# Kernel tuning notes

Hardware: AMD Instinct MI355X
Metric: run time of the kernel (lower is better)

Reference implementation:

```python
import jax, jax.numpy as jnp
import numpy as np
from jax.scipy.special import logsumexp

NEG = -1e9  # soft -inf for log-domain boundaries (avoids NaN grads)


def _viterbi_score(theta, A):
    """Smooth (logsumexp-operator) 3-state affine-gap HMM Viterbi score.

    theta: [B, N, M, 3] emission scores, state order (m, x, y)
    A:     [B, N, M, 3, 3] transition scores A[..., u, v] = u -> v
    Returns per-batch terminal score [B].
    Recurrence:
      V[i,j,m] = theta[i,j,m] + LSE_u(V[i-1,j-1,u] + A[i,j,u,m])
      V[i,j,x] = theta[i,j,x] + LSE_u(V[i-1,j  ,u] + A[i,j,u,x])
      V[i,j,y] = theta[i,j,y] + LSE_u(V[i  ,j-1,u] + A[i,j,u,y])
    The y-state within-row recurrence is a log-domain linear recurrence
    solved with an associative scan (wavefront-free row parallelism).
    """
    B, N, Mlen, S = theta.shape
    dt = theta.dtype

    def combine(e1, e2):
        a1, b1 = e1
        a2, b2 = e2
        return a1 + a2, jnp.logaddexp(b1 + a2, b2)

    # V row over j = 0..M (j=0 is boundary column); start state at (0,0,m)
    V0 = jnp.full((B, Mlen + 1, S), NEG, dt).at[:, 0, 0].set(0.0)
    neg_col = jnp.full((B, 1), NEG, dt)

    def row_step(Vprev, xs):
        th, Aij = xs                      # [B,M,3], [B,M,3,3]
        prev_diag = Vprev[:, :-1]         # V[i-1, j-1, :] for j=1..M
        prev_up = Vprev[:, 1:]            # V[i-1, j,   :]
        Vm = th[..., 0] + logsumexp(prev_diag + Aij[..., 0], axis=-1)
        Vx = th[..., 1] + logsumexp(prev_up + Aij[..., 1], axis=-1)
        # y-state: V_y[j] = logaddexp(a[j] + V_y[j-1], b[j])
        Vm_l = jnp.concatenate([neg_col, Vm[:, :-1]], axis=1)  # V[i,j-1,m]
        Vx_l = jnp.concatenate([neg_col, Vx[:, :-1]], axis=1)  # V[i,j-1,x]
        a = Aij[..., 2, 2] + th[..., 2]
        b = th[..., 2] + jnp.logaddexp(Vm_l + Aij[..., 0, 2],
                                       Vx_l + Aij[..., 1, 2])
        _, Vy = jax.lax.associative_scan(combine, (a, b), axis=1)
        Vrow = jnp.concatenate(
            [jnp.full((B, 1, S), NEG, dt),
             jnp.stack([Vm, Vx, Vy], axis=-1)], axis=1)
        return Vrow, None

    theta_t = jnp.moveaxis(theta, 1, 0)   # [N,B,M,3]
    A_t = jnp.moveaxis(A, 1, 0)           # [N,B,M,3,3]
    Vlast, _ = jax.lax.scan(row_step, V0, (theta_t, A_t))
    return logsumexp(Vlast[:, -1], axis=-1)  # [B]


def setup_inputs() -> dict:
    key = jax.random.key(0)
    ks = jax.random.split(key, 4)
    B, N, M, d, S = 8, 512, 512, 256, 3
    sc = jnp.float32(0.1)
    return {
        "zx": jax.random.normal(ks[0], (B, N, d, S), jnp.float32) * sc,
        "zy": jax.random.normal(ks[1], (B, M, d, S), jnp.float32) * sc,
        "gx": jax.random.normal(ks[2], (B, N, d, S), jnp.float32) * sc,
        "gy": jax.random.normal(ks[3], (B, M, d, S), jnp.float32) * sc,
    }


def reference(zx, zy, gx, gy):
    # HMM3Aligner.contract (no softplus/logsigmoid in the 3-state override)
    theta = jnp.einsum('bids,bjds->bijs', zx, zy)      # [B,N,M,3]
    A = jnp.einsum('bidu,bjdv->bijuv', gx, gy)         # [B,N,M,3,3]
    # hmm.decode: posterior alignment = grad of smooth Viterbi score w.r.t. theta
    aln = jax.grad(lambda th: _viterbi_score(th, A).sum())(theta)
    return aln  # [B,N,M,3]
```

## Files before the change

### kernel.cpp

```cpp
#include <hip/hip_runtime.h>
#include <cstdint>

#define DEVI __device__ __forceinline__

#define NEGC  (-1.0e9f)
#define NEGID (-2.0e9f)

DEVI float lse2f(float p, float q){
  float m = fmaxf(p, q);
  return m + __logf(__expf(p - m) + __expf(q - m));
}
DEVI float lse3f(float a, float b, float c){
  float m = fmaxf(fmaxf(a, b), c);
  return m + __logf(__expf(a - m) + __expf(b - m) + __expf(c - m));
}

DEVI void bar_raw(){
  asm volatile("s_waitcnt lgkmcnt(0)" ::: "memory");
  __builtin_amdgcn_s_barrier();
  asm volatile("" ::: "memory");
}
DEVI void bar_full(){
  asm volatile("s_waitcnt vmcnt(0) lgkmcnt(0)" ::: "memory");
  __builtin_amdgcn_s_barrier();
  asm volatile("" ::: "memory");
}

DEVI void gld_lds16(const float* g, float* l){
  __builtin_amdgcn_global_load_lds(
    (const __attribute__((address_space(1))) unsigned int*)(uintptr_t)g,
    (__attribute__((address_space(3))) unsigned int*)(uintptr_t)l,
    16, 0, 0);
}
DEVI void stage8(const float* g, float* l, int nchunks, int wid, int lane){
  for (int c = wid; c < nchunks; c += 8)
    gld_lds16(g + (size_t)c*256 + lane*4, l + (size_t)c*256);
}

__global__ __launch_bounds__(256) void k_gemm_th(
    const float* __restrict__ zx, const float* __restrict__ zy, float* __restrict__ th){
  const int b  = blockIdx.z;
  const int i0 = blockIdx.y * 64, j0 = blockIdx.x * 64;
  const int tid = threadIdx.x;
  const int tx = tid & 15, ty = tid >> 4;
  __shared__ __align__(16) float xs[16*3*64];
  __shared__ __align__(16) float ys[16*3*64];
  const float* xb = zx + ((size_t)b*512 + i0) * 768;
  const float* yb = zy + ((size_t)b*512 + j0) * 768;
  float acc[3][4][4] = {};
  for (int k = 0; k < 256; k += 16) {
    #pragma unroll
    for (int p = 0; p < 3; ++p) {
      int q = tid + p*256;
      int row = q / 12, f4 = q % 12;
      float4 xv = *(const float4*)(xb + (size_t)row*768 + k*3 + f4*4);
      float4 yv = *(const float4*)(yb + (size_t)row*768 + k*3 + f4*4);
      const float* xe = (const float*)&xv;
      const float* ye = (const float*)&yv;
      #pragma unroll
      for (int e = 0; e < 4; ++e) {
        int idx = f4*4 + e;
        xs[idx*64 + row] = xe[e];
        ys[idx*64 + row] = ye[e];
      }
    }
    __syncthreads();
    #pragma unroll
    for (int dd = 0; dd < 16; ++dd) {
      float4 xa[3], yv2[3];
      #pragma unroll
      for (int s = 0; s < 3; ++s) {
        xa[s]  = *(const float4*)&xs[(dd*3 + s)*64 + ty*4];
        yv2[s] = *(const float4*)&ys[(dd*3 + s)*64 + tx*4];
      }
      #pragma unroll
      for (int s = 0; s < 3; ++s)
        #pragma unroll
        for (int a2 = 0; a2 < 4; ++a2)
          #pragma unroll
          for (int c = 0; c < 4; ++c)
            acc[s][a2][c] += ((const float*)&xa[s])[a2] * ((const float*)&yv2[s])[c];
    }
    __syncthreads();
  }
  #pragma unroll
  for (int s = 0; s < 3; ++s)
    #pragma unroll
    for (int a2 = 0; a2 < 4; ++a2) {
      float4 v = make_float4(acc[s][a2][0], acc[s][a2][1], acc[s][a2][2], acc[s][a2][3]);
      *(float4*)(th + (((size_t)b*512 + i0 + ty*4 + a2)*3 + s)*512 + j0 + tx*4) = v;
    }
}

__global__ __launch_bounds__(256) void k_gemm_A(
    const float* __restrict__ gx, const float* __restrict__ gy, float* __restrict__ Ag){
  const int b  = blockIdx.z;
  const int i0 = blockIdx.y * 32, j0 = blockIdx.x * 32;
  const int tid = threadIdx.x;
  const int tx = tid & 15, ty = tid >> 4;
  __shared__ __align__(16) float xs[32*3*32];
  __shared__ __align__(16) float ys[32*3*32];
  const float* xb = gx + ((size_t)b*512 + i0) * 768;
  const float* yb = gy + ((size_t)b*512 + j0) * 768;
  float acc[3][3][2][2] = {};
  for (int k = 0; k < 256; k += 32) {
    #pragma unroll
    for (int p = 0; p < 3; ++p) {
      int q = tid + p*256;
      int row = q / 24, f4 = q % 24;
      float4 xv = *(const float4*)(xb + (size_t)row*768 + k*3 + f4*4);
      float4 yv = *(const float4*)(yb + (size_t)row*768 + k*3 + f4*4);
      const float* xe = (const float*)&xv;
      const float* ye = (const float*)&yv;
      #pragma unroll
      for (int e = 0; e < 4; ++e) {
        int idx = f4*4 + e;
        xs[idx*32 + row] = xe[e];
        ys[idx*32 + row] = ye[e];
      }
    }
    __syncthreads();
    #pragma unroll
    for (int dd = 0; dd < 32; ++dd) {
      float2 ga[3], gb[3];
      #pragma unroll
      for (int u = 0; u < 3; ++u) ga[u] = *(const float2*)&xs[(dd*3 + u)*32 + ty*2];
      #pragma unroll
      for (int v = 0; v < 3; ++v) gb[v] = *(const float2*)&ys[(dd*3 + v)*32 + tx*2];
      #pragma unroll
      for (int u = 0; u < 3; ++u)
        #pragma unroll
        for (int v = 0; v < 3; ++v) {
          acc[u][v][0][0] += ga[u].x * gb[v].x;
          acc[u][v][0][1] += ga[u].x * gb[v].y;
          acc[u][v][1][0] += ga[u].y * gb[v].x;
          acc[u][v][1][1] += ga[u].y * gb[v].y;
        }
    }
    __syncthreads();
  }
  #pragma unroll
  for (int u = 0; u < 3; ++u)
    #pragma unroll
    for (int v = 0; v < 3; ++v)
      #pragma unroll
      for (int a2 = 0; a2 < 2; ++a2) {
        float2 w; w.x = acc[u][v][a2][0]; w.y = acc[u][v][a2][1];
        *(float2*)(Ag + ((((size_t)b*512 + i0 + ty*2 + a2)*3 + v)*3 + u)*512 + j0 + tx*2) = w;
      }
}

__global__ __launch_bounds__(512) void k_fwd(
    const float* __restrict__ th, const float* __restrict__ Ag,
    float* __restrict__ V, float* __restrict__ score){
  const int b = blockIdx.x;
  const int tid = threadIdx.x;
  const int lane = tid & 63, wid = tid >> 6;
  __shared__ __align__(16) float th_s[2][1536];
  __shared__ __align__(16) float A_s[2][4608];
  __shared__ float Vbuf[2][3*513];
  __shared__ float wag[8][2];
  const float* thb = th + (size_t)b * 512 * 1536;
  const float* Ab  = Ag + (size_t)b * 512 * 4608;
  float*       Vb  = V  + (size_t)b * 512 * 1536;

  for (int kk = tid; kk < 2*3*513; kk += 512) (&Vbuf[0][0])[kk] = NEGC;
  __syncthreads();
  if (tid == 0) Vbuf[0][0] = 0.f;
  stage8(thb, th_s[0], 6, wid, lane);
  stage8(Ab,  A_s[0], 18, wid, lane);
  bar_full();

  int pv = 0;
  for (int i = 1; i <= 512; ++i) {
    const int bc = (i - 1) & 1;
    if (i < 512) {
      stage8(thb + (size_t)i*1536, th_s[i & 1], 6, wid, lane);
      stage8(Ab  + (size_t)i*4608, A_s[i & 1], 18, wid, lane);
    }
    const float* ths = th_s[bc];
    const float* As  = A_s[bc];
    float* Vp = Vbuf[pv];
    float* Vc = Vbuf[pv ^ 1];
    const int tj = tid, j = tid + 1;

    float thm = ths[tj], thx = ths[512 + tj], thy = ths[1024 + tj];
    float vd0 = Vp[tj],     vd1 = Vp[513 + tj],     vd2 = Vp[2*513 + tj];
    float vu0 = Vp[tj + 1], vu1 = Vp[513 + tj + 1], vu2 = Vp[2*513 + tj + 1];
    float Vm = thm + lse3f(vd0 + As[tj],        vd1 + As[512 + tj],  vd2 + As[1024 + tj]);
    float Vx = thx + lse3f(vu0 + As[1536 + tj], vu1 + As[2048 + tj], vu2 + As[2560 + tj]);
    Vc[j] = Vm; Vc[513 + j] = Vx;
    if (tid == 0) { Vc[0] = NEGC; Vc[513] = NEGC; Vc[2*513] = NEGC; }
    bar_raw();
    float Vml = Vc[tj];
    float Vxl = Vc[513 + tj];
    float a  = As[4096 + tj] + thy;
    float bb = thy + lse2f(Vml + As[3072 + tj], Vxl + As[3584 + tj]);
    #pragma unroll
    for (int st = 1; st < 64; st <<= 1) {
      float ao = __shfl_up(a,  st, 64);
      float bo = __shfl_up(bb, st, 64);
      if (lane >= st) { bb = lse2f(bo + a, bb); a += ao; }
    }
    if (lane == 63) { wag[wid][0] = a; wag[wid][1] = bb; }
    bar_raw();
    float pb = NEGID;
    for (int w = 0; w < wid; ++w) pb = lse2f(pb + wag[w][0], wag[w][1]);
    float Vy = lse2f(pb + a, bb);
    Vc[2*513 + j] = Vy;
    float* Vr = Vb + (size_t)(i - 1) * 1536;
    Vr[tj] = Vm; Vr[512 + tj] = Vx; Vr[1024 + tj] = Vy;
    bar_full();
    pv ^= 1;
  }
  if (tid == 0) {
    float* Vl = Vbuf[pv];
    score[b] = lse3f(Vl[512], Vl[513 + 512], Vl[2*513 + 512]);
  }
}

__global__ __launch_bounds__(512) void k_bwd(
    const float* __restrict__ th, const float* __restrict__ Ag,
    const float* __restrict__ V, const float* __restrict__ score,
    float* __restrict__ out){
  const int b = blockIdx.x;
  const int tid = threadIdx.x;
  const int lane = tid & 63, wid = tid >> 6;
  __shared__ __align__(16) float th_s[3][1536];
  __shared__ __align__(16) float A_s[3][4608];
  __shared__ __align__(16) float Vls[3][1536];
  __shared__ float Eb[2][3*514];
  __shared__ float wag[8][2];
  const float* thb = th + (size_t)b * 512 * 1536;
  const float* Ab  = Ag + (size_t)b * 512 * 4608;
  const float* Vb  = V  + (size_t)b * 512 * 1536;
  float* ob = out + (size_t)b * 512 * 512 * 3;

  for (int kk = tid; kk < 2*3*514; kk += 512) (&Eb[0][0])[kk] = 0.f;
  stage8(thb + (size_t)511*1536, th_s[1], 6, wid, lane);
  stage8(Ab  + (size_t)511*4608, A_s[1], 18, wid, lane);
  stage8(Vb  + (size_t)511*1536, Vls[2], 6, wid, lane);
  float sc = score[b];
  bar_full();

  int ce = 0;
  for (int i = 512; i >= 1; --i) {
    if (i >= 2) {
      stage8(thb + (size_t)(i-2)*1536, th_s[(i-2)%3], 6, wid, lane);
      stage8(Ab  + (size_t)(i-2)*4608, A_s[(i-2)%3], 18, wid, lane);
      stage8(Vb  + (size_t)(i-2)*1536, Vls[(i-1)%3], 6, wid, lane);
    }
    const float* thN = th_s[(i-1)%3];
    const float* AN  = A_s[(i-1)%3];
    const float* thK = th_s[i%3];
    const float* AK  = A_s[i%3];
    const float* Vc  = Vls[i%3];
    const float* Vn  = Vls[(i+1)%3];
    const float* E1  = Eb[ce ^ 1];
    float* Ec = Eb[ce];
    const int tj = tid;
    const bool hasN = (i < 512);
    const bool hasJ = (tid < 511);
    const int  c1 = hasJ ? tid + 1 : tid;

    float v0 = Vc[tj], v1 = Vc[512 + tj], v2 = Vc[1024 + tj];
    float vyr = hasJ ? Vc[1024 + c1] : 0.f;
    float vnm = Vn[c1];
    float vnx = Vn[512 + tj];
    float e1m = E1[tid + 2];
    float e1x = E1[514 + tid + 1];
    float thT1 = thK[c1], thT2 = thK[512 + tj], thT3 = thN[1024 + c1];

    float w;
    w = (hasN && hasJ) ? e1m * __expf(v0 + AK[c1]       + thT1 - vnm) : 0.f;
    float D0 = w + (hasN ? e1x * __expf(v0 + AK[1536 + tj] + thT2 - vnx) : 0.f);
    float wy0 = hasJ ? __expf(v0 + AN[3072 + c1] + thT3 - vyr) : 0.f;
    w = (hasN && hasJ) ? e1m * __expf(v1 + AK[512 + c1] + thT1 - vnm) : 0.f;
    float D1 = w + (hasN ? e1x * __expf(v1 + AK[2048 + tj] + thT2 - vnx) : 0.f);
    float wy1 = hasJ ? __expf(v1 + AN[3584 + c1] + thT3 - vyr) : 0.f;
    w = (hasN && hasJ) ? e1m * __expf(v2 + AK[1024 + c1] + thT1 - vnm) : 0.f;
    float D2 = w + (hasN ? e1x * __expf(v2 + AK[2560 + tj] + thT2 - vnx) : 0.f);
    float wy2 = hasJ ? __expf(v2 + AN[4096 + c1] + thT3 - vyr) : 0.f;

    if (i == 512 && tid == 511) {
      D0 = __expf(v0 - sc); D1 = __expf(v1 - sc); D2 = __expf(v2 - sc);
    }

    float ra = wy2;
    float ca = D2;
    #pragma unroll
    for (int st = 1; st < 64; st <<= 1) {
      float ro = __shfl_down(ra, st, 64);
      float co = __shfl_down(ca, st, 64);
      if (lane + st < 64) { ca = ca + ra * co; ra = ra * ro; }
    }
    if (lane == 0) { wag[wid][0] = ra; wag[wid][1] = ca; }
    bar_raw();
    float sr = 1.f, sc2 = 0.f;
    for (int w2 = wid + 1; w2 < 8; ++w2) { sc2 = sc2 + sr * wag[w2][1]; sr = sr * wag[w2][0]; }
    float Ey = ca + ra * sc2;
    Ec[2*514 + tid + 1] = Ey;
    bar_raw();
    float EyR = Ec[2*514 + tid + 2];
    float Em = D0 + wy0 * EyR;
    float Ex = D1 + wy1 * EyR;
    Ec[tid + 1] = Em;
    Ec[514 + tid + 1] = Ex;
    float* o = ob + ((size_t)(i - 1) * 512 + tj) * 3;
    o[0] = Em; o[1] = Ex; o[2] = Ey;
    bar_full();
    ce ^= 1;
  }
}

extern "C" void kernel_launch(void* const* d_in, const int* in_sizes, int n_in,
                              void* d_out, int out_size, void* d_ws, size_t ws_size,
                              hipStream_t stream) {
  const float* zx = (const float*)d_in[0];
  const float* zy = (const float*)d_in[1];
  const float* gx = (const float*)d_in[2];
  const float* gy = (const float*)d_in[3];
  float* ws = (float*)d_ws;
  float* th = ws;
  float* Ag = ws + 6291456;
  float* V  = ws + 25165824;
  float* sc = ws + 31457280;
  float* out = (float*)d_out;

  k_gemm_th<<<dim3(8, 8, 8),   256, 0, stream>>>(zx, zy, th);
  k_gemm_A <<<dim3(16, 16, 8), 256, 0, stream>>>(gx, gy, Ag);
  k_fwd<<<8, 512, 0, stream>>>(th, Ag, V, sc);
  k_bwd<<<8, 512, 0, stream>>>(th, Ag, V, sc, out);
}
```

Measured before the change: 2.481 ms.

## Remove intra-row barriers via shuffles and defer global row stores

In the forward kernel, the left-neighbour Vm/Vx values now come from a wavefront shuffle, and lane 0 recomputes its left neighbour, replacing an LDS round-trip and barrier. In the backward kernel, the right-neighbour Ey is derived from a shuffle of the scan partials plus the suffix carry, removing the Ey LDS store and a barrier. Both kernels defer each row's global output stores to the next iteration so the stores overlap the following row's work instead of being drained by the end-of-row full barrier. The cost is some redundant lane-0 compute and a few extra live registers.

```diff
diff --git a/kernel.cpp b/kernel.cpp
--- a/kernel.cpp
+++ b/kernel.cpp
@@ -159,7 +159,7 @@
   __shared__ __align__(16) float th_s[2][1536];
   __shared__ __align__(16) float A_s[2][4608];
   __shared__ float Vbuf[2][3*513];
-  __shared__ float wag[8][2];
+  __shared__ __align__(8) float wag[8][2];
   const float* thb = th + (size_t)b * 512 * 1536;
   const float* Ab  = Ag + (size_t)b * 512 * 4608;
   float*       Vb  = V  + (size_t)b * 512 * 1536;
@@ -171,29 +171,42 @@
   stage8(Ab,  A_s[0], 18, wid, lane);
   bar_full();
 
+  float pVm = NEGC, pVx = NEGC, pVy = NEGC;
   int pv = 0;
   for (int i = 1; i <= 512; ++i) {
-    const int bc = (i - 1) & 1;
+    if (i > 1) {
+      float* Vr = Vb + (size_t)(i - 2) * 1536;
+      Vr[tid] = pVm; Vr[512 + tid] = pVx; Vr[1024 + tid] = pVy;
+    }
     if (i < 512) {
       stage8(thb + (size_t)i*1536, th_s[i & 1], 6, wid, lane);
       stage8(Ab  + (size_t)i*4608, A_s[i & 1], 18, wid, lane);
     }
-    const float* ths = th_s[bc];
-    const float* As  = A_s[bc];
+    const float* ths = th_s[(i - 1) & 1];
+    const float* As  = A_s[(i - 1) & 1];
     float* Vp = Vbuf[pv];
     float* Vc = Vbuf[pv ^ 1];
     const int tj = tid, j = tid + 1;
 
-    float thm = ths[tj], thx = ths[512 + tj], thy = ths[1024 + tj];
     float vd0 = Vp[tj],     vd1 = Vp[513 + tj],     vd2 = Vp[2*513 + tj];
     float vu0 = Vp[tj + 1], vu1 = Vp[513 + tj + 1], vu2 = Vp[2*513 + tj + 1];
-    float Vm = thm + lse3f(vd0 + As[tj],        vd1 + As[512 + tj],  vd2 + As[1024 + tj]);
-    float Vx = thx + lse3f(vu0 + As[1536 + tj], vu1 + As[2048 + tj], vu2 + As[2560 + tj]);
+    float Vm = ths[tj]       + lse3f(vd0 + As[tj],        vd1 + As[512 + tj],  vd2 + As[1024 + tj]);
+    float Vx = ths[512 + tj] + lse3f(vu0 + As[1536 + tj], vu1 + As[2048 + tj], vu2 + As[2560 + tj]);
+    float Vml = __shfl_up(Vm, 1, 64);
+    float Vxl = __shfl_up(Vx, 1, 64);
+    if (lane == 0) {
+      if (tid == 0) { Vml = NEGC; Vxl = NEGC; }
+      else {
+        int q = tj - 1;
+        float e0 = Vp[q], e1 = Vp[513 + q], e2 = Vp[2*513 + q];
+        float f0 = Vp[q + 1], f1 = Vp[513 + q + 1], f2 = Vp[2*513 + q + 1];
+        Vml = ths[q]       + lse3f(e0 + As[q],        e1 + As[512 + q],  e2 + As[1024 + q]);
+        Vxl = ths[512 + q] + lse3f(f0 + As[1536 + q], f1 + As[2048 + q], f2 + As[2560 + q]);
+      }
+    }
     Vc[j] = Vm; Vc[513 + j] = Vx;
     if (tid == 0) { Vc[0] = NEGC; Vc[513] = NEGC; Vc[2*513] = NEGC; }
-    bar_raw();
-    float Vml = Vc[tj];
-    float Vxl = Vc[513 + tj];
+    float thy = ths[1024 + tj];
     float a  = As[4096 + tj] + thy;
     float bb = thy + lse2f(Vml + As[3072 + tj], Vxl + As[3584 + tj]);
     #pragma unroll
@@ -208,15 +221,13 @@
     for (int w = 0; w < wid; ++w) pb = lse2f(pb + wag[w][0], wag[w][1]);
     float Vy = lse2f(pb + a, bb);
     Vc[2*513 + j] = Vy;
-    float* Vr = Vb + (size_t)(i - 1) * 1536;
-    Vr[tj] = Vm; Vr[512 + tj] = Vx; Vr[1024 + tj] = Vy;
+    pVm = Vm; pVx = Vx; pVy = Vy;
     bar_full();
     pv ^= 1;
   }
-  if (tid == 0) {
-    float* Vl = Vbuf[pv];
-    score[b] = lse3f(Vl[512], Vl[513 + 512], Vl[2*513 + 512]);
-  }
+  float* Vr = Vb + (size_t)511 * 1536;
+  Vr[tid] = pVm; Vr[512 + tid] = pVx; Vr[1024 + tid] = pVy;
+  if (tid == 511) score[b] = lse3f(pVm, pVx, pVy);
 }
 
 __global__ __launch_bounds__(512) void k_bwd(
@@ -229,22 +240,27 @@
   __shared__ __align__(16) float th_s[3][1536];
   __shared__ __align__(16) float A_s[3][4608];
   __shared__ __align__(16) float Vls[3][1536];
-  __shared__ float Eb[2][3*514];
-  __shared__ float wag[8][2];
+  __shared__ float Eb[2][2*514];
+  __shared__ __align__(8) float wag[8][2];
   const float* thb = th + (size_t)b * 512 * 1536;
   const float* Ab  = Ag + (size_t)b * 512 * 4608;
   const float* Vb  = V  + (size_t)b * 512 * 1536;
   float* ob = out + (size_t)b * 512 * 512 * 3;
 
-  for (int kk = tid; kk < 2*3*514; kk += 512) (&Eb[0][0])[kk] = 0.f;
+  for (int kk = tid; kk < 2*2*514; kk += 512) (&Eb[0][0])[kk] = 0.f;
   stage8(thb + (size_t)511*1536, th_s[1], 6, wid, lane);
   stage8(Ab  + (size_t)511*4608, A_s[1], 18, wid, lane);
   stage8(Vb  + (size_t)511*1536, Vls[2], 6, wid, lane);
   float sc = score[b];
   bar_full();
 
+  float pEm = 0.f, pEx = 0.f, pEy = 0.f;
   int ce = 0;
   for (int i = 512; i >= 1; --i) {
+    if (i < 512) {
+      float* o = ob + ((size_t)i * 512 + tid) * 3;
+      o[0] = pEm; o[1] = pEx; o[2] = pEy;
+    }
     if (i >= 2) {
       stage8(thb + (size_t)(i-2)*1536, th_s[(i-2)%3], 6, wid, lane);
       stage8(Ab  + (size_t)(i-2)*4608, A_s[(i-2)%3], 18, wid, lane);
@@ -286,8 +302,7 @@
       D0 = __expf(v0 - sc); D1 = __expf(v1 - sc); D2 = __expf(v2 - sc);
     }
 
-    float ra = wy2;
-    float ca = D2;
+    float ra = wy2, ca = D2;
     #pragma unroll
     for (int st = 1; st < 64; st <<= 1) {
       float ro = __shfl_down(ra, st, 64);
@@ -296,21 +311,28 @@
     }
     if (lane == 0) { wag[wid][0] = ra; wag[wid][1] = ca; }
     bar_raw();
-    float sr = 1.f, sc2 = 0.f;
-    for (int w2 = wid + 1; w2 < 8; ++w2) { sc2 = sc2 + sr * wag[w2][1]; sr = sr * wag[w2][0]; }
-    float Ey = ca + ra * sc2;
-    Ec[2*514 + tid + 1] = Ey;
-    bar_raw();
-    float EyR = Ec[2*514 + tid + 2];
+    float sr = 1.f, s2 = 0.f;
+    #pragma unroll
+    for (int w2 = 0; w2 < 8; ++w2) {
+      if (w2 > wid) {
+        float2 wv = *(const float2*)&wag[w2][0];
+        s2 = s2 + sr * wv.y; sr = sr * wv.x;
+      }
+    }
+    float Ey = ca + ra * s2;
+    float co2 = __shfl_down(ca, 1, 64);
+    float ro2 = __shfl_down(ra, 1, 64);
+    float EyR = (lane == 63) ? s2 : (co2 + ro2 * s2);
     float Em = D0 + wy0 * EyR;
     float Ex = D1 + wy1 * EyR;
     Ec[tid + 1] = Em;
     Ec[514 + tid + 1] = Ex;
-    float* o = ob + ((size_t)(i - 1) * 512 + tj) * 3;
-    o[0] = Em; o[1] = Ex; o[2] = Ey;
+    pEm = Em; pEx = Ex; pEy = Ey;
     bar_full();
     ce ^= 1;
   }
+  float* o = ob + (size_t)tid * 3;
+  o[0] = pEm; o[1] = pEx; o[2] = pEy;
 }
 
 extern "C" void kernel_launch(void* const* d_in, const int* in_sizes, int n_in,
```

After: 2.406 ms. 1.03x faster.
